# Performance work log

Measured on AMD Instinct MI355X. Metric: run time of the kernel, lower is better.

The kernel has to match this reference:

```python
import jax, jax.numpy as jnp
import numpy as np

D_MODEL = 1024   # 'seq_len' arg = input feature dim
FF_DIM = 1024
SCALE = 0.03125  # 1/sqrt(1024)


def setup_inputs() -> dict:
    key = jax.random.key(0)
    ks = jax.random.split(key, 7)
    B, T = 8, 2048
    s = 1.0 / np.sqrt(D_MODEL)
    return {
        "sequence": jax.random.normal(ks[0], (B, T, D_MODEL), dtype=jnp.float32),
        "Wq": jax.random.uniform(ks[1], (FF_DIM, D_MODEL), jnp.float32, -s, s),
        "bq": jax.random.uniform(ks[2], (FF_DIM,), jnp.float32, -s, s),
        "Wk": jax.random.uniform(ks[3], (FF_DIM, D_MODEL), jnp.float32, -s, s),
        "bk": jax.random.uniform(ks[4], (FF_DIM,), jnp.float32, -s, s),
        "Wv": jax.random.uniform(ks[5], (FF_DIM, D_MODEL), jnp.float32, -s, s),
        "bv": jax.random.uniform(ks[6], (FF_DIM,), jnp.float32, -s, s),
    }


def reference(sequence, Wq, bq, Wk, bk, Wv, bv):
    # Q/K/V linear projections (torch Linear: x @ W.T + b)
    q = jnp.einsum('btd,fd->btf', sequence, Wq) + bq
    k = jnp.einsum('btd,fd->btf', sequence, Wk) + bk
    v = jnp.einsum('btd,fd->btf', sequence, Wv) + bv
    # scaled dot-product attention (dropout p=0 -> identity)
    scores = jnp.einsum('btf,bsf->bts', q, k) * SCALE  # [B,T,T]
    attn = jax.nn.softmax(scores, axis=-1)
    return jnp.einsum('bts,bsf->btf', attn, v)
```

## Files before the change

kernel.cpp:

```cpp
#include <hip/hip_runtime.h>
#include <hip/hip_bf16.h>

#define BB 8
#define TT 2048
#define DD 1024
#define FF 1024

typedef __attribute__((ext_vector_type(8))) short bf16x8;
typedef __attribute__((ext_vector_type(4))) float f32x4;
typedef __attribute__((ext_vector_type(4))) short s16x4;

constexpr float kScaleLog2e = 0.03125f * 1.44269504088896340736f;

__device__ __forceinline__ short bf16_bits(float x) {
    __hip_bfloat16 h = __float2bfloat16(x);
    short s;
    __builtin_memcpy(&s, &h, sizeof(short));
    return s;
}

__global__ __launch_bounds__(256) void cvt_all(
    const float* __restrict__ seq, const float* __restrict__ Wq,
    const float* __restrict__ Wk, const float* __restrict__ Wv,
    short* __restrict__ seqb, short* __restrict__ Wb)
{
    const int bid = blockIdx.x;
    const float* src;
    short* dst;
    int i;
    if (bid < 8192)      { src = seq; dst = seqb;                      i = bid * 256 + threadIdx.x; }
    else if (bid < 8704) { src = Wq;  dst = Wb;                        i = (bid - 8192) * 256 + threadIdx.x; }
    else if (bid < 9216) { src = Wk;  dst = Wb + (size_t)FF * DD;      i = (bid - 8704) * 256 + threadIdx.x; }
    else                 { src = Wv;  dst = Wb + (size_t)2 * FF * DD;  i = (bid - 9216) * 256 + threadIdx.x; }
    f32x4 a = ((const f32x4*)src)[2 * i];
    f32x4 b = ((const f32x4*)src)[2 * i + 1];
    bf16x8 o;
#pragma unroll
    for (int j = 0; j < 4; ++j) { o[j] = bf16_bits(a[j]); o[4 + j] = bf16_bits(b[j]); }
    ((bf16x8*)dst)[i] = o;
}

__device__ __forceinline__ void gemm_core(
    const short* __restrict__ A, int lda, int m0,
    const short* __restrict__ B, int ldb, int n0,
    int K, short* As, short* Bs, f32x4 acc[4][4])
{
    const int tid  = threadIdx.x;
    const int lane = tid & 63;
    const int w    = tid >> 6;
    const int wm   = (w & 1) * 64;
    const int wn   = (w >> 1) * 64;
    const int r    = lane & 15;
    const int qd   = lane >> 4;

    for (int k0 = 0; k0 < K; k0 += 32) {
        __syncthreads();
#pragma unroll
        for (int it = 0; it < 2; ++it) {
            const int s   = tid + it * 256;
            const int row = s >> 2;
            const int cg  = ((s & 3) - (row >> 1)) & 3;
            const int col = cg << 3;
            __builtin_amdgcn_global_load_lds(
                (const __attribute__((address_space(1))) unsigned int*)
                    (A + (size_t)(m0 + row) * lda + k0 + col),
                (__attribute__((address_space(3))) unsigned int*)(As + s * 8),
                16, 0, 0);
            __builtin_amdgcn_global_load_lds(
                (const __attribute__((address_space(1))) unsigned int*)
                    (B + (size_t)(n0 + row) * ldb + k0 + col),
                (__attribute__((address_space(3))) unsigned int*)(Bs + s * 8),
                16, 0, 0);
        }
        __syncthreads();
        bf16x8 af[4], bf[4];
#pragma unroll
        for (int m = 0; m < 4; ++m) {
            const int R = wm + m * 16 + r;
            af[m] = *(const bf16x8*)(As + R * 32 + (((qd + (R >> 1)) & 3) << 3));
        }
#pragma unroll
        for (int n = 0; n < 4; ++n) {
            const int R = wn + n * 16 + r;
            bf[n] = *(const bf16x8*)(Bs + R * 32 + (((qd + (R >> 1)) & 3) << 3));
        }
#pragma unroll
        for (int m = 0; m < 4; ++m)
#pragma unroll
            for (int n = 0; n < 4; ++n)
                acc[m][n] = __builtin_amdgcn_mfma_f32_16x16x32_bf16(af[m], bf[n], acc[m][n], 0, 0, 0);
    }
}

__global__ __launch_bounds__(256) void qkv_tiled(
    const short* __restrict__ seqb, const short* __restrict__ Wb,
    const float* __restrict__ bq, const float* __restrict__ bk,
    const float* __restrict__ bv,
    __hip_bfloat16* __restrict__ q, __hip_bfloat16* __restrict__ k,
    __hip_bfloat16* __restrict__ vT)
{
    __shared__ short As[128 * 32], Bs[128 * 32];
    const int bid  = blockIdx.x;
    const int mt   = bid / 24;
    const int rest = bid % 24;
    const int nt   = rest & 7;
    const int proj = rest >> 3;

    const short* W    = Wb + (size_t)proj * FF * DD;
    const float* bias = proj == 0 ? bq : (proj == 1 ? bk : bv);

    f32x4 acc[4][4];
#pragma unroll
    for (int m = 0; m < 4; ++m)
#pragma unroll
        for (int n = 0; n < 4; ++n) acc[m][n] = (f32x4){0.f, 0.f, 0.f, 0.f};

    gemm_core(seqb, DD, mt * 128, W, DD, nt * 128, DD, As, Bs, acc);

    const int lane = threadIdx.x & 63;
    const int w    = threadIdx.x >> 6;
    const int wm   = (w & 1) * 64;
    const int wn   = (w >> 1) * 64;
    const int r    = lane & 15;
    const int qd   = lane >> 4;
    const int row_base = mt * 128 + wm + qd * 4;
    const int col_base = nt * 128 + wn + r;

    if (proj < 2) {
        __hip_bfloat16* dst = (proj == 0) ? q : k;
#pragma unroll
        for (int n = 0; n < 4; ++n) {
            const int col = col_base + n * 16;
            const float bv_ = bias[col];
#pragma unroll
            for (int m = 0; m < 4; ++m)
#pragma unroll
                for (int i = 0; i < 4; ++i)
                    dst[(size_t)(row_base + m * 16 + i) * FF + col] =
                        __float2bfloat16(acc[m][n][i] + bv_);
        }
    } else {
#pragma unroll
        for (int m = 0; m < 4; ++m) {
            const int rowg = row_base + m * 16;
            const int b_   = rowg >> 11;
            const int t_   = rowg & 2047;
            __hip_bfloat16* vb = vT + (size_t)b_ * FF * TT;
#pragma unroll
            for (int n = 0; n < 4; ++n) {
                const int col = col_base + n * 16;
                const float bv_ = bias[col];
                s16x4 pack;
#pragma unroll
                for (int i = 0; i < 4; ++i) pack[i] = bf16_bits(acc[m][n][i] + bv_);
                *(s16x4*)(vb + (size_t)col * TT + t_) = pack;
            }
        }
    }
}

__global__ __launch_bounds__(256) void score_tiled(
    const __hip_bfloat16* __restrict__ q, const __hip_bfloat16* __restrict__ k,
    __hip_bfloat16* __restrict__ P, float* __restrict__ Z)
{
    __shared__ short As[128 * 32], Bs[128 * 32];
    const int bid = blockIdx.x;
    const int b   = bid >> 8;
    const int rem = bid & 255;
    const int tt  = rem >> 4;
    const int st  = rem & 15;

    const short* qb = (const short*)q + (size_t)b * TT * FF;
    const short* kb = (const short*)k + (size_t)b * TT * FF;

    f32x4 acc[4][4];
#pragma unroll
    for (int m = 0; m < 4; ++m)
#pragma unroll
        for (int n = 0; n < 4; ++n) acc[m][n] = (f32x4){0.f, 0.f, 0.f, 0.f};

    gemm_core(qb, FF, tt * 128, kb, FF, st * 128, FF, As, Bs, acc);

    const int lane = threadIdx.x & 63;
    const int w    = threadIdx.x >> 6;
    const int wm   = (w & 1) * 64;
    const int wn   = (w >> 1) * 64;
    const int r    = lane & 15;
    const int qd   = lane >> 4;
    const int row_base = tt * 128 + wm + qd * 4;
    const int col_base = st * 128 + wn + r;

    __hip_bfloat16* Pb = P + (size_t)b * TT * TT;
    float* Zb = Z + b * TT;

    float rs[4][4];
#pragma unroll
    for (int m = 0; m < 4; ++m)
#pragma unroll
        for (int i = 0; i < 4; ++i) rs[m][i] = 0.f;

#pragma unroll
    for (int m = 0; m < 4; ++m)
#pragma unroll
        for (int n = 0; n < 4; ++n) {
            const int col = col_base + n * 16;
#pragma unroll
            for (int i = 0; i < 4; ++i) {
                const float e = exp2f(acc[m][n][i] * kScaleLog2e);
                const __hip_bfloat16 eb = __float2bfloat16(e);
                rs[m][i] += __bfloat162float(eb);
                Pb[(size_t)(row_base + m * 16 + i) * TT + col] = eb;
            }
        }
#pragma unroll
    for (int off = 1; off < 16; off <<= 1)
#pragma unroll
        for (int m = 0; m < 4; ++m)
#pragma unroll
            for (int i = 0; i < 4; ++i) rs[m][i] += __shfl_xor(rs[m][i], off, 64);
    if (r == 0) {
#pragma unroll
        for (int m = 0; m < 4; ++m)
#pragma unroll
            for (int i = 0; i < 4; ++i)
                atomicAdd(&Zb[row_base + m * 16 + i], rs[m][i]);
    }
}

__global__ __launch_bounds__(256) void pv_tiled(
    const __hip_bfloat16* __restrict__ P, const __hip_bfloat16* __restrict__ vT,
    const float* __restrict__ Z, float* __restrict__ out)
{
    __shared__ short As[128 * 32], Bs[128 * 32];
    const int bid = blockIdx.x;
    const int b   = bid >> 7;
    const int rem = bid & 127;
    const int tt  = rem >> 3;
    const int ft  = rem & 7;

    const short* Pb = (const short*)P + (size_t)b * TT * TT;
    const short* vb = (const short*)vT + (size_t)b * FF * TT;

    f32x4 acc[4][4];
#pragma unroll
    for (int m = 0; m < 4; ++m)
#pragma unroll
        for (int n = 0; n < 4; ++n) acc[m][n] = (f32x4){0.f, 0.f, 0.f, 0.f};

    gemm_core(Pb, TT, tt * 128, vb, TT, ft * 128, TT, As, Bs, acc);

    const int lane = threadIdx.x & 63;
    const int w    = threadIdx.x >> 6;
    const int wm   = (w & 1) * 64;
    const int wn   = (w >> 1) * 64;
    const int r    = lane & 15;
    const int qd   = lane >> 4;
    const int row_base = tt * 128 + wm + qd * 4;
    const int col_base = ft * 128 + wn + r;

    const float* Zb = Z + b * TT;
    float* ob = out + (size_t)b * TT * FF;

#pragma unroll
    for (int m = 0; m < 4; ++m) {
        float rz[4];
#pragma unroll
        for (int i = 0; i < 4; ++i) rz[i] = 1.0f / Zb[row_base + m * 16 + i];
#pragma unroll
        for (int n = 0; n < 4; ++n) {
            const int col = col_base + n * 16;
#pragma unroll
            for (int i = 0; i < 4; ++i)
                ob[(size_t)(row_base + m * 16 + i) * FF + col] = acc[m][n][i] * rz[i];
        }
    }
}

extern "C" void kernel_launch(void* const* d_in, const int* in_sizes, int n_in,
                              void* d_out, int out_size, void* d_ws, size_t ws_size,
                              hipStream_t stream) {
    const float* seq = (const float*)d_in[0];
    const float* Wq  = (const float*)d_in[1];
    const float* bq  = (const float*)d_in[2];
    const float* Wk  = (const float*)d_in[3];
    const float* bk  = (const float*)d_in[4];
    const float* Wv  = (const float*)d_in[5];
    const float* bv  = (const float*)d_in[6];
    float* out = (float*)d_out;
    char* ws = (char*)d_ws;

    const size_t MB32 = 33554432;
    __hip_bfloat16* q   = (__hip_bfloat16*)(ws);
    __hip_bfloat16* k   = (__hip_bfloat16*)(ws + MB32);
    __hip_bfloat16* vT  = (__hip_bfloat16*)(ws + 2 * MB32);
    __hip_bfloat16* P   = (__hip_bfloat16*)(ws + 3 * MB32);
    float*          Z   = (float*)(ws + 3 * MB32 + (size_t)67108864);
    short*          seqb = (short*)P;
    short*          Wb   = (short*)((char*)P + MB32);

    hipMemsetAsync(Z, 0, (size_t)BB * TT * sizeof(float), stream);

    cvt_all<<<9728, 256, 0, stream>>>(seq, Wq, Wk, Wv, seqb, Wb);
    qkv_tiled<<<128 * 24, 256, 0, stream>>>(seqb, Wb, bq, bk, bv, q, k, vT);
    score_tiled<<<BB * 256, 256, 0, stream>>>(q, k, P, Z);
    pv_tiled<<<BB * 128, 256, 0, stream>>>(P, vT, Z, out);
}
```

Measured before the change: 454.5 us.

## Triple-buffer GEMM tiles with LDS flag-based warp sync and fold Z memset into conversion

Replaces the two-barrier-per-k-step GEMM loop with a three-stage ring of LDS tiles. Each wave issues its own async global-to-LDS loads two steps ahead and synchronises through per-buffer ready/done counters in LDS, polled with s_sleep, instead of __syncthreads. The Z zeroing memset is folded into extra blocks of the conversion kernel to remove one launch. LDS use per block triples, which may lower occupancy, and the spin-wait protocol depends on correct vmcnt accounting across waves.

```diff
diff --git a/kernel.cpp b/kernel.cpp
--- a/kernel.cpp
+++ b/kernel.cpp
@@ -22,9 +22,14 @@
 __global__ __launch_bounds__(256) void cvt_all(
     const float* __restrict__ seq, const float* __restrict__ Wq,
     const float* __restrict__ Wk, const float* __restrict__ Wv,
-    short* __restrict__ seqb, short* __restrict__ Wb)
+    short* __restrict__ seqb, short* __restrict__ Wb, float* __restrict__ Z)
 {
     const int bid = blockIdx.x;
+    if (bid >= 9728) {
+        const int i = (bid - 9728) * 1024 + threadIdx.x * 4;
+        *(f32x4*)(Z + i) = (f32x4){0.f, 0.f, 0.f, 0.f};
+        return;
+    }
     const float* src;
     short* dst;
     int i;
@@ -40,10 +45,34 @@
     ((bf16x8*)dst)[i] = o;
 }
 
-__device__ __forceinline__ void gemm_core(
+__device__ __forceinline__ void issue_tile(
     const short* __restrict__ A, int lda, int m0,
     const short* __restrict__ B, int ldb, int n0,
-    int K, short* As, short* Bs, f32x4 acc[4][4])
+    int k0, short* buf , int w, int lane)
+{
+#pragma unroll
+    for (int it = 0; it < 2; ++it) {
+        const int s   = w * 64 + it * 256 + lane;
+        const int row = s >> 2;
+        const int cg  = ((s & 3) - (row >> 1)) & 3;
+        const int col = cg << 3;
+        __builtin_amdgcn_global_load_lds(
+            (const __attribute__((address_space(1))) unsigned int*)
+                (A + (size_t)(m0 + row) * lda + k0 + col),
+            (__attribute__((address_space(3))) unsigned int*)(buf + s * 8),
+            16, 0, 0);
+        __builtin_amdgcn_global_load_lds(
+            (const __attribute__((address_space(1))) unsigned int*)
+                (B + (size_t)(n0 + row) * ldb + k0 + col),
+            (__attribute__((address_space(3))) unsigned int*)(buf + 4096 + s * 8),
+            16, 0, 0);
+    }
+}
+
+__device__ __forceinline__ void gemm_core_async(
+    const short* __restrict__ A, int lda, int m0,
+    const short* __restrict__ B, int ldb, int n0,
+    int K, short* tiles, int* flags, f32x4 acc[4][4])
 {
     const int tid  = threadIdx.x;
     const int lane = tid & 63;
@@ -52,28 +81,41 @@
     const int wn   = (w >> 1) * 64;
     const int r    = lane & 15;
     const int qd   = lane >> 4;
-
-    for (int k0 = 0; k0 < K; k0 += 32) {
-        __syncthreads();
-#pragma unroll
-        for (int it = 0; it < 2; ++it) {
-            const int s   = tid + it * 256;
-            const int row = s >> 2;
-            const int cg  = ((s & 3) - (row >> 1)) & 3;
-            const int col = cg << 3;
-            __builtin_amdgcn_global_load_lds(
-                (const __attribute__((address_space(1))) unsigned int*)
-                    (A + (size_t)(m0 + row) * lda + k0 + col),
-                (__attribute__((address_space(3))) unsigned int*)(As + s * 8),
-                16, 0, 0);
-            __builtin_amdgcn_global_load_lds(
-                (const __attribute__((address_space(1))) unsigned int*)
-                    (B + (size_t)(n0 + row) * ldb + k0 + col),
-                (__attribute__((address_space(3))) unsigned int*)(Bs + s * 8),
-                16, 0, 0);
-        }
-        __syncthreads();
-        bf16x8 af[4], bf[4];
+    int* ready = flags;
+    int* done  = flags + 4;
+
+    if (tid < 8) flags[tid] = 0;
+    __syncthreads();
+
+    const int T = K >> 5;
+    issue_tile(A, lda, m0, B, ldb, n0, 0,  tiles,        w, lane);
+    issue_tile(A, lda, m0, B, ldb, n0, 32, tiles + 8192, w, lane);
+
+    for (int k = 0; k < T; ++k) {
+        const int bk = k % 3;
+        const int j  = k + 2;
+        if (j < T) {
+            const int bj = j % 3;
+            if (j >= 3) {
+                const int tgt = 4 * (j / 3);
+                while (*(volatile int*)&done[bj] < tgt) __builtin_amdgcn_s_sleep(1);
+            }
+            asm volatile("" ::: "memory");
+            issue_tile(A, lda, m0, B, ldb, n0, j << 5, tiles + bj * 8192, w, lane);
+        }
+        if (j < T)          asm volatile("s_waitcnt vmcnt(8)" ::: "memory");
+        else if (k + 1 < T) asm volatile("s_waitcnt vmcnt(4)" ::: "memory");
+        else                asm volatile("s_waitcnt vmcnt(0)" ::: "memory");
+        if (lane == 0) atomicAdd(&ready[bk], 1);
+        {
+            const int tgt = 4 * (k / 3 + 1);
+            while (*(volatile int*)&ready[bk] < tgt) __builtin_amdgcn_s_sleep(1);
+        }
+        asm volatile("" ::: "memory");
+
+        const short* As = tiles + bk * 8192;
+        const short* Bs = As + 4096;
+        bf16x8 af[4], bf4[4];
 #pragma unroll
         for (int m = 0; m < 4; ++m) {
             const int R = wm + m * 16 + r;
@@ -82,15 +124,20 @@
 #pragma unroll
         for (int n = 0; n < 4; ++n) {
             const int R = wn + n * 16 + r;
-            bf[n] = *(const bf16x8*)(Bs + R * 32 + (((qd + (R >> 1)) & 3) << 3));
+            bf4[n] = *(const bf16x8*)(Bs + R * 32 + (((qd + (R >> 1)) & 3) << 3));
         }
 #pragma unroll
         for (int m = 0; m < 4; ++m)
 #pragma unroll
             for (int n = 0; n < 4; ++n)
-                acc[m][n] = __builtin_amdgcn_mfma_f32_16x16x32_bf16(af[m], bf[n], acc[m][n], 0, 0, 0);
-    }
-}
+                acc[m][n] = __builtin_amdgcn_mfma_f32_16x16x32_bf16(af[m], bf4[n], acc[m][n], 0, 0, 0);
+
+        asm volatile("" ::: "memory");
+        if (lane == 0) atomicAdd(&done[bk], 1);
+    }
+}
+
+#define GEMM_SMEM __shared__ short tiles[3 * 8192]; __shared__ int flags[8];
 
 __global__ __launch_bounds__(256) void qkv_tiled(
     const short* __restrict__ seqb, const short* __restrict__ Wb,
@@ -99,7 +146,7 @@
     __hip_bfloat16* __restrict__ q, __hip_bfloat16* __restrict__ k,
     __hip_bfloat16* __restrict__ vT)
 {
-    __shared__ short As[128 * 32], Bs[128 * 32];
+    GEMM_SMEM
     const int bid  = blockIdx.x;
     const int mt   = bid / 24;
     const int rest = bid % 24;
@@ -115,7 +162,7 @@
 #pragma unroll
         for (int n = 0; n < 4; ++n) acc[m][n] = (f32x4){0.f, 0.f, 0.f, 0.f};
 
-    gemm_core(seqb, DD, mt * 128, W, DD, nt * 128, DD, As, Bs, acc);
+    gemm_core_async(seqb, DD, mt * 128, W, DD, nt * 128, DD, tiles, flags, acc);
 
     const int lane = threadIdx.x & 63;
     const int w    = threadIdx.x >> 6;
@@ -163,7 +210,7 @@
     const __hip_bfloat16* __restrict__ q, const __hip_bfloat16* __restrict__ k,
     __hip_bfloat16* __restrict__ P, float* __restrict__ Z)
 {
-    __shared__ short As[128 * 32], Bs[128 * 32];
+    GEMM_SMEM
     const int bid = blockIdx.x;
     const int b   = bid >> 8;
     const int rem = bid & 255;
@@ -179,7 +226,7 @@
 #pragma unroll
         for (int n = 0; n < 4; ++n) acc[m][n] = (f32x4){0.f, 0.f, 0.f, 0.f};
 
-    gemm_core(qb, FF, tt * 128, kb, FF, st * 128, FF, As, Bs, acc);
+    gemm_core_async(qb, FF, tt * 128, kb, FF, st * 128, FF, tiles, flags, acc);
 
     const int lane = threadIdx.x & 63;
     const int w    = threadIdx.x >> 6;
@@ -231,7 +278,7 @@
     const __hip_bfloat16* __restrict__ P, const __hip_bfloat16* __restrict__ vT,
     const float* __restrict__ Z, float* __restrict__ out)
 {
-    __shared__ short As[128 * 32], Bs[128 * 32];
+    GEMM_SMEM
     const int bid = blockIdx.x;
     const int b   = bid >> 7;
     const int rem = bid & 127;
@@ -247,7 +294,7 @@
 #pragma unroll
         for (int n = 0; n < 4; ++n) acc[m][n] = (f32x4){0.f, 0.f, 0.f, 0.f};
 
-    gemm_core(Pb, TT, tt * 128, vb, TT, ft * 128, TT, As, Bs, acc);
+    gemm_core_async(Pb, TT, tt * 128, vb, TT, ft * 128, TT, tiles, flags, acc);
 
     const int lane = threadIdx.x & 63;
     const int w    = threadIdx.x >> 6;
@@ -298,9 +345,7 @@
     short*          seqb = (short*)P;
     short*          Wb   = (short*)((char*)P + MB32);
 
-    hipMemsetAsync(Z, 0, (size_t)BB * TT * sizeof(float), stream);
-
-    cvt_all<<<9728, 256, 0, stream>>>(seq, Wq, Wk, Wv, seqb, Wb);
+    cvt_all<<<9744, 256, 0, stream>>>(seq, Wq, Wk, Wv, seqb, Wb, Z);
     qkv_tiled<<<128 * 24, 256, 0, stream>>>(seqb, Wb, bq, bk, bv, q, k, vT);
     score_tiled<<<BB * 256, 256, 0, stream>>>(q, k, P, Z);
     pv_tiled<<<BB * 128, 256, 0, stream>>>(P, vT, Z, out);
```

Result: slower. 501.0 us (+10.2%).
